# Performance work log

Measured on AMD Instinct MI355X. Metric: run time of the kernel, lower is better.

The kernel has to match this reference:

```python
import jax, jax.numpy as jnp
import numpy as np

B, D, TX, TY = 32, 192, 256, 1024
NEG = -1e9


def setup_inputs() -> dict:
    key = jax.random.key(0)
    k1, k2, k3, k4 = jax.random.split(key, 4)
    x = jax.random.normal(k1, (B, D, TX), jnp.float32)
    y = jax.random.normal(k2, (B, D, TY), jnp.float32)
    # ensure 1 <= x_lens <= TX <= y_lens <= TY so a monotonic path exists
    x_lens = jax.random.randint(k3, (B,), 64, TX + 1, jnp.int32)
    y_lens = jax.random.randint(k4, (B,), 512, TY + 1, jnp.int32)
    return {"x": x, "x_lens": x_lens, "y": y, "y_lens": y_lens}


def _log_prior(x, y):
    # Gaussian log-prior: factor = -0.5 everywhere, so
    # log_prior[b,t,s] = -0.5*sum_d y^2 + sum_d x*y - 0.5*sum_d x^2 + const
    ndim = x.shape[1]
    const = jnp.asarray(-0.5 * np.log(2.0 * np.pi) * ndim, x.dtype)
    y_sq = -0.5 * jnp.sum(y * y, axis=1)            # [B, TY]
    x_sq = -0.5 * jnp.sum(x * x, axis=1)            # [B, TX]
    xy = jnp.einsum('bdt,bds->bts', x, y)           # [B, TX, TY]
    return y_sq[:, None, :] + xy + x_sq[:, :, None] + const


def _maximum_path(log_prior, x_lens, y_lens):
    # Viterbi-style monotonic alignment search (Glow-TTS / VITS maximum_path).
    b, tx, ty = log_prior.shape
    xr = jnp.arange(tx)

    # --- forward DP over mel frames (columns of the (tx, ty) grid) ---
    col0 = jnp.where(xr[None, :] == 0, log_prior[:, :, 0], NEG)  # [B, TX]

    def fwd(prev, inp):
        lp_col, yi = inp                               # lp_col: [B, TX]
        v_cur = jnp.where(xr[None, :] == yi, NEG, prev)
        v_prev = jnp.concatenate(
            [jnp.full((b, 1), NEG, prev.dtype), prev[:, :-1]], axis=1)
        cur = lp_col + jnp.maximum(v_cur, v_prev)
        return cur, cur

    lp_t = jnp.moveaxis(log_prior, 2, 0)               # [TY, B, TX]
    _, cols = jax.lax.scan(fwd, col0, (lp_t[1:], jnp.arange(1, ty)))
    value = jnp.concatenate([col0[None], cols], axis=0)  # [TY, B, TX]

    # value at column y-1 (dummy at y=0, never used for the decision there)
    vprev = jnp.concatenate([value[:1], value[:-1]], axis=0)

    # --- backtrack from (x_lens-1, y_lens-1) down to y=0 ---
    def bwd(index, inp):
        yi, vpc = inp                                  # vpc: [B, TX]
        active = yi < y_lens                           # [B]
        row = jnp.where(active[:, None],
                        jax.nn.one_hot(index, tx, dtype=log_prior.dtype), 0.0)
        vm1 = jnp.take_along_axis(
            vpc, jnp.maximum(index - 1, 0)[:, None], axis=1)[:, 0]
        v0 = jnp.take_along_axis(vpc, index[:, None], axis=1)[:, 0]
        move = (index != 0) & ((index == yi) | (vm1 > v0)) & active
        return index - move.astype(index.dtype), row

    idx0 = x_lens - 1
    _, rows = jax.lax.scan(bwd, idx0, (jnp.arange(ty), vprev), reverse=True)
    return jnp.moveaxis(rows, 0, 2)                    # [B, TX, TY]


def reference(x, x_lens, y, y_lens):
    log_prior = _log_prior(x, y)
    attn = _maximum_path(log_prior, x_lens, y_lens)
    return jax.lax.stop_gradient(attn)
```

## Files before the change

kernel.cpp:

```cpp
#include <hip/hip_runtime.h>
#include <stdint.h>

#define B_  32
#define D_  192
#define TX_ 256
#define TY_ 1024
#define NEGV -1e9f
#define LPCONST ((float)(-176.43619837529715))

__global__ __launch_bounds__(256) void k0_sq(const float* __restrict__ x,
                                             const float* __restrict__ y,
                                             float* __restrict__ xsq,
                                             float* __restrict__ ysq) {
    int gid = blockIdx.x * 256 + threadIdx.x;
    if (gid < B_ * TX_) {
        int b = gid >> 8, t = gid & 255;
        const float* p = x + (size_t)b * D_ * TX_ + t;
        float s = 0.f;
        #pragma unroll 8
        for (int d = 0; d < D_; ++d) { float v = p[(size_t)d * TX_]; s += v * v; }
        xsq[gid] = -0.5f * s;
    } else {
        int g = gid - B_ * TX_;
        int b = g >> 10, t = g & 1023;
        const float* p = y + (size_t)b * D_ * TY_ + t;
        float s = 0.f;
        #pragma unroll 8
        for (int d = 0; d < D_; ++d) { float v = p[(size_t)d * TY_]; s += v * v; }
        ysq[g] = -0.5f * s;
    }
}

#define BT 128
#define BS 128
#define BK 32
__global__ __launch_bounds__(256) void k1_gemm(const float* __restrict__ x,
                                               const float* __restrict__ y,
                                               const float* __restrict__ xsq,
                                               const float* __restrict__ ysq,
                                               float* __restrict__ lp) {
    __shared__ float xs[BK][BT];
    __shared__ float ys[BK][BS];
    const int id = blockIdx.x;
    const int r  = id & 7;
    const int g  = id >> 3;
    const int b  = r + 8 * (g >> 4);
    const int sub = g & 15;
    const int t0 = (sub >> 3) * BT;
    const int s0 = (sub & 7) * BS;
    const int tid = threadIdx.x;
    const int ti = tid & 15;
    const int si = tid >> 4;

    float acc[8][8];
    #pragma unroll
    for (int i = 0; i < 8; ++i)
        #pragma unroll
        for (int j = 0; j < 8; ++j) acc[i][j] = 0.f;

    const float* xg = x + (size_t)b * D_ * TX_ + t0;
    const float* yg = y + (size_t)b * D_ * TY_ + s0;

    for (int k0 = 0; k0 < D_; k0 += BK) {
        #pragma unroll
        for (int i = 0; i < 4; ++i) {
            int f = tid + i * 256;
            int row = f >> 5;
            int col = (f & 31) * 4;
            float4 v = *(const float4*)(xg + (size_t)(k0 + row) * TX_ + col);
            *(float4*)&xs[row][col] = v;
            float4 w = *(const float4*)(yg + (size_t)(k0 + row) * TY_ + col);
            *(float4*)&ys[row][col] = w;
        }
        __syncthreads();
        #pragma unroll
        for (int k = 0; k < BK; ++k) {
            float xr[8], yr[8];
            *(float4*)&xr[0] = *(float4*)&xs[k][ti * 8];
            *(float4*)&xr[4] = *(float4*)&xs[k][ti * 8 + 4];
            *(float4*)&yr[0] = *(float4*)&ys[k][si * 8];
            *(float4*)&yr[4] = *(float4*)&ys[k][si * 8 + 4];
            #pragma unroll
            for (int i = 0; i < 8; ++i)
                #pragma unroll
                for (int j = 0; j < 8; ++j) acc[i][j] += xr[i] * yr[j];
        }
        __syncthreads();
    }

    float xq[8], yq[8];
    *(float4*)&xq[0] = *(const float4*)(xsq + b * TX_ + t0 + ti * 8);
    *(float4*)&xq[4] = *(const float4*)(xsq + b * TX_ + t0 + ti * 8 + 4);
    *(float4*)&yq[0] = *(const float4*)(ysq + b * TY_ + s0 + si * 8);
    *(float4*)&yq[4] = *(const float4*)(ysq + b * TY_ + s0 + si * 8 + 4);

    #pragma unroll
    for (int js = 0; js < 8; ++js) {
        float* op = lp + (size_t)(b * TY_ + s0 + si * 8 + js) * TX_ + t0 + ti * 8;
        float o[8];
        #pragma unroll
        for (int it = 0; it < 8; ++it) {
            float v = yq[js] + acc[it][js];
            v = v + xq[it];
            o[it] = v + LPCONST;
        }
        *(float4*)op       = *(float4*)&o[0];
        *(float4*)(op + 4) = *(float4*)&o[4];
    }
}

__global__ __launch_bounds__(64) void k2_dp(const float* __restrict__ lp,
                                            const int* __restrict__ xlens,
                                            const int* __restrict__ ylens,
                                            unsigned char* __restrict__ path) {
    __shared__ unsigned int RB[TX_][33];
    __shared__ unsigned int PTw[TY_ / 4];
    unsigned char* PT = (unsigned char*)PTw;

    const int b = blockIdx.x;
    const int l = threadIdx.x;
    const int xlen = xlens[b];
    const int ylen = ylens[b];
    const int send = (ylen + 31) & ~31;
    const float* base = lp + (size_t)b * TY_ * TX_ + l * 4;
    const int tt0 = l * 4;

#define LDCOL(s) (*(const float4*)(base + (size_t)(((s) < TY_) ? (s) : (TY_ - 1)) * TX_))

#define PROC(s, fv, PRE) {                                              \
    unsigned int sbit = 1u << ((s) & 31);                               \
    bool e0 = false, e1 = false, e2 = false, e3 = false;                \
    if (PRE) { e0 = (tt0 == (s));     e1 = (tt0 + 1 == (s));            \
               e2 = (tt0 + 2 == (s)); e3 = (tt0 + 3 == (s)); }          \
    if ((l != 0) && (e0 || (shv > p0))) rw0 |= sbit;                    \
    if (e1 || (p0 > p1)) rw1 |= sbit;                                   \
    if (e2 || (p1 > p2)) rw2 |= sbit;                                   \
    if (e3 || (p2 > p3)) rw3 |= sbit;                                   \
    float c3 = (fv).w + fmaxf(e3 ? NEGV : p3, p2);                      \
    float nsh = __shfl_up(c3, 1);                                       \
    float c2 = (fv).z + fmaxf(e2 ? NEGV : p2, p1);                      \
    float c1 = (fv).y + fmaxf(e1 ? NEGV : p1, p0);                      \
    float c0 = (fv).x + fmaxf(e0 ? NEGV : p0, (l == 0) ? NEGV : shv);   \
    p0 = c0; p1 = c1; p2 = c2; p3 = c3; shv = nsh;                      \
}

#define FLUSH(w) { RB[tt0][w] = rw0; RB[tt0 + 1][w] = rw1;              \
                   RB[tt0 + 2][w] = rw2; RB[tt0 + 3][w] = rw3;          \
                   rw0 = rw1 = rw2 = rw3 = 0; }

    float4 g[16];
    #pragma unroll
    for (int i = 0; i < 16; ++i) g[i] = LDCOL(i);

    float p0, p1, p2, p3, shv;
    unsigned int rw0 = 0, rw1 = 0, rw2 = 0, rw3 = 0;

    p0 = (l == 0) ? g[0].x : NEGV;
    p1 = NEGV; p2 = NEGV; p3 = NEGV;
    shv = NEGV;
    g[0] = LDCOL(16);

    #pragma unroll
    for (int j = 1; j < 16; ++j) { PROC(j, g[j], true) g[j] = LDCOL(16 + j); }

    #pragma unroll 1
    for (int sb = 16; sb < 256; sb += 16) {
        #pragma unroll
        for (int j = 0; j < 16; ++j) { PROC(sb + j, g[j], true) g[j] = LDCOL(sb + 16 + j); }
        if (((sb + 15) & 31) == 31) FLUSH((sb + 15) >> 5)
    }
    #pragma unroll 1
    for (int sb = 256; sb < send; sb += 16) {
        #pragma unroll
        for (int j = 0; j < 16; ++j) { PROC(sb + j, g[j], false) g[j] = LDCOL(sb + 16 + j); }
        if (((sb + 15) & 31) == 31) FLUSH((sb + 15) >> 5)
    }
    __syncthreads();

    if (l == 0) {
        int idx = xlen - 1;
        int yi = ylen - 1;
        while (yi >= 0) {
            int w = yi >> 5;
            unsigned int cur = RB[idx][w] & (0xFFFFFFFFu >> (31 - (yi & 31)));
            int lo; bool mv;
            if (cur) { lo = (w << 5) + (31 - __clz(cur)); mv = true; }
            else     { lo = (w << 5);                      mv = false; }
            for (int q = lo; q <= yi; ++q) PT[q] = (unsigned char)idx;
            if (mv) --idx;
            yi = lo - 1;
        }
    }
    __syncthreads();
    {
        unsigned int* pd = (unsigned int*)(path + b * TY_);
        #pragma unroll
        for (int k = 0; k < 4; ++k) pd[l + k * 64] = PTw[l + k * 64];
    }
}

__global__ __launch_bounds__(256) void k3_out(const unsigned char* __restrict__ path,
                                              const int* __restrict__ ylens,
                                              float* __restrict__ out) {
    int F = blockIdx.x * 256 + threadIdx.x;
    int yi = (F & 255) * 4;
    int t  = (F >> 8) & 255;
    int b  = F >> 16;
    int ylen = ylens[b];
    unsigned int pw = *(const unsigned int*)(path + b * TY_ + yi);
    float4 v;
    v.x = (((pw      ) & 255u) == (unsigned)t && yi     < ylen) ? 1.f : 0.f;
    v.y = (((pw >>  8) & 255u) == (unsigned)t && yi + 1 < ylen) ? 1.f : 0.f;
    v.z = (((pw >> 16) & 255u) == (unsigned)t && yi + 2 < ylen) ? 1.f : 0.f;
    v.w = (((pw >> 24) & 255u) == (unsigned)t && yi + 3 < ylen) ? 1.f : 0.f;
    ((float4*)out)[F] = v;
}

extern "C" void kernel_launch(void* const* d_in, const int* in_sizes, int n_in,
                              void* d_out, int out_size, void* d_ws, size_t ws_size,
                              hipStream_t stream) {
    const float* x  = (const float*)d_in[0];
    const int*   xl = (const int*)d_in[1];
    const float* y  = (const float*)d_in[2];
    const int*   yl = (const int*)d_in[3];
    float* out = (float*)d_out;

    char* ws = (char*)d_ws;
    float* xsq = (float*)ws;
    float* ysq = (float*)(ws + 32 * 1024);
    unsigned char* path = (unsigned char*)(ws + 160 * 1024);

    float* lp = out;

    k0_sq  <<<160, 256, 0, stream>>>(x, y, xsq, ysq);
    k1_gemm<<<512, 256, 0, stream>>>(x, y, xsq, ysq, lp);
    k2_dp  <<<B_, 64, 0, stream>>>(lp, xl, yl, path);
    k3_out <<<(B_ * TX_ * TY_ / 4) / 256, 256, 0, stream>>>(path, yl, out);
}
```

Measured before the change: 185.5 us.

## Stream DP columns through an LDS ring via async global_load_lds prefetch

Replaces the register-held 16-column prefetch in the serial DP kernel with a 64-slot LDS ring buffer filled by global_load_lds, keeping 56 columns in flight and gating each step on vmcnt. Each column is then read from LDS into a small register rotation of 8. The backtrack loop is also restructured to cache the current and next-row bitmask words so fewer LDS reads sit on the serial path. This deepens memory latency hiding for the latency-bound single-wave DP, at the cost of a large LDS footprint (64 KB ring) and a per-column waitcnt that may serialize issue.

```diff
diff --git a/kernel.cpp b/kernel.cpp
--- a/kernel.cpp
+++ b/kernel.cpp
@@ -109,10 +109,20 @@
     }
 }
 
-__global__ __launch_bounds__(64) void k2_dp(const float* __restrict__ lp,
-                                            const int* __restrict__ xlens,
-                                            const int* __restrict__ ylens,
-                                            unsigned char* __restrict__ path) {
+#define DPD 56
+#define RSLOTS 64
+
+__device__ __forceinline__ void gload16(const float* gp, float* lp_) {
+    __builtin_amdgcn_global_load_lds(
+        (const __attribute__((address_space(1))) unsigned int*)(gp),
+        (__attribute__((address_space(3))) unsigned int*)(lp_), 16, 0, 0);
+}
+
+__global__ __launch_bounds__(64, 1) void k2_dp(const float* __restrict__ lp,
+                                               const int* __restrict__ xlens,
+                                               const int* __restrict__ ylens,
+                                               unsigned char* __restrict__ path) {
+    __shared__ float ring[RSLOTS * 256];
     __shared__ unsigned int RB[TX_][33];
     __shared__ unsigned int PTw[TY_ / 4];
     unsigned char* PT = (unsigned char*)PTw;
@@ -122,10 +132,34 @@
     const int xlen = xlens[b];
     const int ylen = ylens[b];
     const int send = (ylen + 31) & ~31;
-    const float* base = lp + (size_t)b * TY_ * TX_ + l * 4;
+    const float* gl = lp + (size_t)b * TY_ * TX_ + l * 4;
     const int tt0 = l * 4;
 
-#define LDCOL(s) (*(const float4*)(base + (size_t)(((s) < TY_) ? (s) : (TY_ - 1)) * TX_))
+    #pragma unroll 1
+    for (int i = 0; i <= DPD; ++i) {
+        int sc = i;
+        gload16(gl + (size_t)sc * TX_, &ring[(i & (RSLOTS - 1)) * 256]);
+    }
+    asm volatile("s_waitcnt vmcnt(48)" ::: "memory");
+    __builtin_amdgcn_sched_barrier(0);
+
+    float4 rr0, rr1, rr2, rr3, rr4, rr5, rr6, rr7;
+    rr0 = *(float4*)&ring[0 * 256 + l * 4];
+    rr1 = *(float4*)&ring[1 * 256 + l * 4];
+    rr2 = *(float4*)&ring[2 * 256 + l * 4];
+    rr3 = *(float4*)&ring[3 * 256 + l * 4];
+    rr4 = *(float4*)&ring[4 * 256 + l * 4];
+    rr5 = *(float4*)&ring[5 * 256 + l * 4];
+    rr6 = *(float4*)&ring[6 * 256 + l * 4];
+    rr7 = *(float4*)&ring[7 * 256 + l * 4];
+
+    float p0, p1, p2, p3, shv;
+    unsigned int rw0 = 0, rw1 = 0, rw2 = 0, rw3 = 0;
+
+    p0 = (l == 0) ? rr0.x : NEGV;
+    p1 = NEGV; p2 = NEGV; p3 = NEGV;
+    shv = NEGV;
+    rr0 = *(float4*)&ring[8 * 256 + l * 4];
 
 #define PROC(s, fv, PRE) {                                              \
     unsigned int sbit = 1u << ((s) & 31);                               \
@@ -148,47 +182,82 @@
                    RB[tt0 + 2][w] = rw2; RB[tt0 + 3][w] = rw3;          \
                    rw0 = rw1 = rw2 = rw3 = 0; }
 
-    float4 g[16];
-    #pragma unroll
-    for (int i = 0; i < 16; ++i) g[i] = LDCOL(i);
-
-    float p0, p1, p2, p3, shv;
-    unsigned int rw0 = 0, rw1 = 0, rw2 = 0, rw3 = 0;
-
-    p0 = (l == 0) ? g[0].x : NEGV;
-    p1 = NEGV; p2 = NEGV; p3 = NEGV;
-    shv = NEGV;
-    g[0] = LDCOL(16);
-
-    #pragma unroll
-    for (int j = 1; j < 16; ++j) { PROC(j, g[j], true) g[j] = LDCOL(16 + j); }
+#define COLBODY(s, rr, PRE) {                                           \
+    int sc = (s) + DPD; if (sc > TY_ - 1) sc = TY_ - 1;                 \
+    gload16(gl + (size_t)sc * TX_,                                      \
+            &ring[(((s) + DPD) & (RSLOTS - 1)) * 256]);                 \
+    asm volatile("s_waitcnt vmcnt(48)" ::: "memory");                   \
+    __builtin_amdgcn_sched_barrier(0);                                  \
+    float4 nf = *(float4*)&ring[((((s) + 8) & (RSLOTS - 1)) * 256) + l * 4]; \
+    PROC(s, rr, PRE)                                                    \
+    rr = nf;                                                            \
+}
+
+    COLBODY(1, rr1, true)
+    COLBODY(2, rr2, true)
+    COLBODY(3, rr3, true)
+    COLBODY(4, rr4, true)
+    COLBODY(5, rr5, true)
+    COLBODY(6, rr6, true)
+    COLBODY(7, rr7, true)
 
     #pragma unroll 1
-    for (int sb = 16; sb < 256; sb += 16) {
-        #pragma unroll
-        for (int j = 0; j < 16; ++j) { PROC(sb + j, g[j], true) g[j] = LDCOL(sb + 16 + j); }
-        if (((sb + 15) & 31) == 31) FLUSH((sb + 15) >> 5)
+    for (int sb = 8; sb < 256; sb += 8) {
+        COLBODY(sb + 0, rr0, true)
+        COLBODY(sb + 1, rr1, true)
+        COLBODY(sb + 2, rr2, true)
+        COLBODY(sb + 3, rr3, true)
+        COLBODY(sb + 4, rr4, true)
+        COLBODY(sb + 5, rr5, true)
+        COLBODY(sb + 6, rr6, true)
+        COLBODY(sb + 7, rr7, true)
+        if (((sb + 7) & 31) == 31) FLUSH((sb + 7) >> 5)
     }
     #pragma unroll 1
-    for (int sb = 256; sb < send; sb += 16) {
-        #pragma unroll
-        for (int j = 0; j < 16; ++j) { PROC(sb + j, g[j], false) g[j] = LDCOL(sb + 16 + j); }
-        if (((sb + 15) & 31) == 31) FLUSH((sb + 15) >> 5)
+    for (int sb = 256; sb < send; sb += 8) {
+        COLBODY(sb + 0, rr0, false)
+        COLBODY(sb + 1, rr1, false)
+        COLBODY(sb + 2, rr2, false)
+        COLBODY(sb + 3, rr3, false)
+        COLBODY(sb + 4, rr4, false)
+        COLBODY(sb + 5, rr5, false)
+        COLBODY(sb + 6, rr6, false)
+        COLBODY(sb + 7, rr7, false)
+        if (((sb + 7) & 31) == 31) FLUSH((sb + 7) >> 5)
     }
     __syncthreads();
 
     if (l == 0) {
         int idx = xlen - 1;
         int yi = ylen - 1;
+        int w = yi >> 5;
+        unsigned int cur = RB[idx][w];
+        unsigned int below = (idx > 0) ? RB[idx - 1][w] : 0u;
         while (yi >= 0) {
-            int w = yi >> 5;
-            unsigned int cur = RB[idx][w] & (0xFFFFFFFFu >> (31 - (yi & 31)));
-            int lo; bool mv;
-            if (cur) { lo = (w << 5) + (31 - __clz(cur)); mv = true; }
-            else     { lo = (w << 5);                      mv = false; }
-            for (int q = lo; q <= yi; ++q) PT[q] = (unsigned char)idx;
-            if (mv) --idx;
-            yi = lo - 1;
+            unsigned int m = cur & (0xFFFFFFFFu >> (31 - (yi & 31)));
+            if (m) {
+                int hb = 31 - __clz(m);
+                int lo = (w << 5) + hb;
+                for (int q = lo; q <= yi; ++q) PT[q] = (unsigned char)idx;
+                --idx;
+                cur = below;
+                below = (idx > 0) ? RB[idx - 1][w] : 0u;
+                yi = lo - 1;
+                if (yi >= 0 && (yi >> 5) < w) {
+                    w = yi >> 5;
+                    cur = RB[idx][w];
+                    below = (idx > 0) ? RB[idx - 1][w] : 0u;
+                }
+            } else {
+                int lo = w << 5;
+                for (int q = lo; q <= yi; ++q) PT[q] = (unsigned char)idx;
+                yi = lo - 1;
+                if (yi >= 0) {
+                    --w;
+                    cur = RB[idx][w];
+                    below = (idx > 0) ? RB[idx - 1][w] : 0u;
+                }
+            }
         }
     }
     __syncthreads();
```

Result: slower. 372.9 us (+101.0%).
